# Kernel tuning notes

Measured on AMD Instinct MI355X. Metric: run time of the kernel, lower is better.

Reference implementation:

```python
import jax, jax.numpy as jnp
import numpy as np

N, E, L = 2048, 16384, 8
IN_DIM, HID, PE, EDGE_DIM, OUT_DIM, HEADS, MASK_DIM = 9, 256, 20, 2, 6, 8, 6
ENC = HID - PE
HD = HID // HEADS

def _bn(x, g, b):
    # BatchNorm1d in training-mode math (batch statistics, biased var), dropout disabled
    mu = x.mean(0)
    var = ((x - mu) ** 2).mean(0)
    return (x - mu) * jax.lax.rsqrt(var + 1e-5) * g + b

def _leaky(x):
    return jnp.where(x > 0, x, 0.01 * x)

def setup_inputs():
    key = jax.random.key(0)
    ks = iter(jax.random.split(key, 64))
    def p(*shape):
        return jax.random.normal(next(ks), shape, jnp.float32) * 0.05
    return dict(
        x=jax.random.normal(next(ks), (N, IN_DIM), jnp.float32),
        pe=jax.random.normal(next(ks), (N, PE), jnp.float32),
        edge_attr=jax.random.normal(next(ks), (E, EDGE_DIM), jnp.float32),
        mask_value=jax.random.normal(next(ks), (MASK_DIM,), jnp.float32),
        enc_w=p(IN_DIM, ENC), enc_b=p(ENC),
        in_g=jnp.ones((ENC,)), in_b=jnp.zeros((ENC,)),
        pe_g=jnp.ones((PE,)), pe_b=jnp.zeros((PE,)),
        gine_ew=p(L, EDGE_DIM, HID), gine_eb=p(L, HID),
        gine_mw=p(L, HID, HID), gine_mb=p(L, HID),
        attn_inw=p(L, HID, 3 * HID), attn_inb=p(L, 3 * HID),
        attn_outw=p(L, HID, HID), attn_outb=p(L, HID),
        mlp1w=p(L, HID, 2 * HID), mlp1b=p(L, 2 * HID),
        mlp2w=p(L, 2 * HID, HID), mlp2b=p(L, HID),
        n1g=jnp.ones((L, HID)), n1b=jnp.zeros((L, HID)),
        n2g=jnp.ones((L, HID)), n2b=jnp.zeros((L, HID)),
        n3g=jnp.ones((L, HID)), n3b=jnp.zeros((L, HID)),
        obn_g=jnp.ones((L, HID)), obn_b=jnp.zeros((L, HID)),
        pd_g=jnp.ones((HID,)), pd_b=jnp.zeros((HID,)),
        dec1w=p(HID, HID), dec1b=p(HID),
        dec2w=p(HID, OUT_DIM), dec2b=p(OUT_DIM),
        edge_index=jax.random.randint(next(ks), (2, E), 0, N, jnp.int32),
        mask=jax.random.randint(next(ks), (N, MASK_DIM), 0, 2, jnp.int32).astype(bool),
    )

def reference(x, pe, edge_attr, mask_value, enc_w, enc_b, in_g, in_b, pe_g, pe_b,
              gine_ew, gine_eb, gine_mw, gine_mb, attn_inw, attn_inb, attn_outw, attn_outb,
              mlp1w, mlp1b, mlp2w, mlp2b, n1g, n1b, n2g, n2b, n3g, n3b, obn_g, obn_b,
              pd_g, pd_b, dec1w, dec1b, dec2w, dec2b, edge_index, mask):
    src, dst = edge_index[0], edge_index[1]
    # masked-feature replacement on x[:, 3:3+mask_dim]
    blk = jnp.where(mask, mask_value[None, :], x[:, 3:3 + MASK_DIM])
    x = x.at[:, 3:3 + MASK_DIM].set(blk)
    h = _bn(_leaky(x @ enc_w + enc_b), in_g, in_b)
    h = jnp.concatenate([h, _bn(pe, pe_g, pe_b)], axis=1)  # [N, HID]
    for l in range(L):
        xin = h
        # GINEConv (eps=0): nn((1+eps)*x_i + sum_j relu(x_j + lin(e_ji)))
        eemb = edge_attr @ gine_ew[l] + gine_eb[l]            # [E, HID]
        msg = jax.nn.relu(xin[src] + eemb)                    # gather + fuse
        agg = jax.ops.segment_sum(msg, dst, num_segments=N)   # scatter-add
        hl = _leaky((xin + agg) @ gine_mw[l] + gine_mb[l])
        hl = _bn(hl + xin, n1g[l], n1b[l])                    # local branch + residual + norm1
        # global multi-head self-attention (single graph -> dense batch, no padding)
        qkv = xin @ attn_inw[l] + attn_inb[l]
        q, k, v = [t.reshape(N, HEADS, HD) for t in jnp.split(qkv, 3, axis=1)]
        a = jax.nn.softmax(jnp.einsum('nhd,mhd->hnm', q, k) / np.float32(np.sqrt(HD)), axis=-1)
        o = jnp.einsum('hnm,mhd->nhd', a, v).reshape(N, HID)
        ha = _bn(o @ attn_outw[l] + attn_outb[l] + xin, n2g[l], n2b[l])  # attn branch + residual + norm2
        out = hl + ha
        out = out + (jax.nn.relu(out @ mlp1w[l] + mlp1b[l]) @ mlp2w[l] + mlp2b[l])  # GPS FFN
        out = _bn(out, n3g[l], n3b[l])
        h = _bn(out, obn_g[l], obn_b[l])                      # outer per-layer BatchNorm
    h = _bn(h, pd_g, pd_b)
    return _leaky(h @ dec1w + dec1b) @ dec2w + dec2b
```

## Files before the change

kernel.cpp:

```cpp
#include <hip/hip_runtime.h>
#include <hip/hip_bf16.h>

typedef __hip_bfloat16 bf16;
typedef __attribute__((ext_vector_type(8))) short v8s;
typedef __attribute__((ext_vector_type(4))) float v4f;

#define NN 2048
#define EE 16384
#define LLAYERS 8
#define HIDD 256
#define ENCD 236
#define PED 20
#define BN_EPS 1e-5f
#define ATT_SCALE 0.17677669529663687f
#define KSPLIT 4

__device__ __forceinline__ float b2f(bf16 v){ return __bfloat162float(v); }
__device__ __forceinline__ float bs2f(unsigned short u){ return __uint_as_float(((unsigned)u) << 16); }
__device__ __forceinline__ unsigned short f2bs(float f){
  bf16 h = __float2bfloat16(f);
  union { bf16 b; unsigned short u; } cv; cv.b = h; return cv.u;
}
__device__ __forceinline__ float ld1f(const void* p, size_t i, int f){
  return f ? b2f(((const bf16*)p)[i]) : ((const float*)p)[i];
}

__global__ void k_detect2(const unsigned int* __restrict__ xw,
                          const unsigned char* __restrict__ mk, int* __restrict__ flags){
  __shared__ int sh[256];
  int t = threadIdx.x;
  if (blockIdx.x == 0){
    int cnt = 0;
    for (int i = t; i < 8192; i += 256){
      unsigned b = (xw[i] >> 8) & 0xffu;
      unsigned v = b & 0x7fu;
      if (v == 0u || (v >= 0x30u && v <= 0x43u)) cnt++;
    }
    sh[t] = cnt; __syncthreads();
    for (int s = 128; s; s >>= 1){ if (t < s) sh[t] += sh[t+s]; __syncthreads(); }
    if (t == 0) flags[0] = (sh[0] > 6000) ? 1 : 0;
  } else {
    int acc = 0;
    for (int i = t; i < NN*6; i += 256){
      unsigned b = mk[i]; int m = i & 3;
      if ((m == 1 && b == 0x3Fu) || (m == 0 && b == 0x80u)) acc |= 4;
      if (b == 0x3Fu || b == 0x80u) acc |= 2;
      if (m != 0 && b != 0u) acc |= 1;
    }
    sh[t] = acc; __syncthreads();
    for (int s = 128; s; s >>= 1){ if (t < s) sh[t] |= sh[t+s]; __syncthreads(); }
    if (t == 0){
      int a = sh[0];
      flags[1] = (a & 4) ? 2 : (a & 2) ? 3 : (a & 1) ? 1 : 0;
    }
  }
}

__global__ void k_tw(const void* __restrict__ src, unsigned short* __restrict__ dst,
                     int K, int N, const int* __restrict__ dflag){
  __shared__ float tile[32][33];
  int n0 = blockIdx.x*32, k0 = blockIdx.y*32, b = blockIdx.z;
  int t = threadIdx.x, x = t & 31, y = t >> 5;
  int f = dflag[0];
  size_t so = (size_t)b*K*N, dofs = (size_t)b*N*K;
  #pragma unroll
  for (int i = 0; i < 4; i++){
    int k = k0 + y + 8*i;
    tile[y+8*i][x] = ld1f(src, so + (size_t)k*N + n0 + x, f);
  }
  __syncthreads();
  #pragma unroll
  for (int i = 0; i < 4; i++){
    int n = n0 + y + 8*i;
    dst[dofs + (size_t)n*K + k0 + x] = f2bs(tile[x][y+8*i]);
  }
}
__global__ void k_tw3(const void* __restrict__ sA, const void* __restrict__ sB,
                      const void* __restrict__ sC, unsigned short* __restrict__ dst,
                      const int* __restrict__ dflag){
  __shared__ float tile[32][33];
  int z = blockIdx.z;
  const void* src = (z < 8) ? sA : (z < 16) ? sB : sC;
  int b = (z < 8) ? z : (z < 16) ? z - 8 : 0;
  int n0 = blockIdx.x*32, k0 = blockIdx.y*32;
  int t = threadIdx.x, x = t & 31, y = t >> 5;
  int f = dflag[0];
  size_t so = (size_t)b*65536, dofs = (size_t)z*65536;
  #pragma unroll
  for (int i = 0; i < 4; i++){
    int k = k0 + y + 8*i;
    tile[y+8*i][x] = ld1f(src, so + (size_t)k*256 + n0 + x, f);
  }
  __syncthreads();
  #pragma unroll
  for (int i = 0; i < 4; i++){
    int n = n0 + y + 8*i;
    dst[dofs + (size_t)n*256 + k0 + x] = f2bs(tile[x][y+8*i]);
  }
}

__global__ void k_csr_count(const int* __restrict__ ei, int* __restrict__ counts){
  int e = blockIdx.x*256 + threadIdx.x;
  if (e < EE) atomicAdd(&counts[ei[EE + e]], 1);
}
__global__ void k_csr_scan(const int* __restrict__ counts, int* __restrict__ rowstart,
                           int* __restrict__ cursor){
  __shared__ int ts[256];
  int t = threadIdx.x, base = t*8;
  int loc[8]; int s = 0;
  #pragma unroll
  for (int i = 0; i < 8; i++){ loc[i] = s; s += counts[base + i]; }
  ts[t] = s; __syncthreads();
  for (int off = 1; off < 256; off <<= 1){
    int v = (t >= off) ? ts[t - off] : 0;
    __syncthreads();
    ts[t] += v;
    __syncthreads();
  }
  int excl = ts[t] - s;
  #pragma unroll
  for (int i = 0; i < 8; i++){
    int v = excl + loc[i];
    rowstart[base + i] = v; cursor[base + i] = v;
  }
  if (t == 255) rowstart[2048] = ts[255];
}
__global__ void k_csr_fill(const int* __restrict__ ei, const void* __restrict__ ea,
                           const int* __restrict__ dflag, int* __restrict__ cursor,
                           int* __restrict__ csr_src, float2* __restrict__ csr_a){
  int e = blockIdx.x*256 + threadIdx.x;
  if (e >= EE) return;
  int s = ei[e], d = ei[EE + e];
  int pos = atomicAdd(&cursor[d], 1);
  int f = dflag[0];
  csr_src[pos] = s;
  csr_a[pos] = make_float2(ld1f(ea, (size_t)e*2, f), ld1f(ea, (size_t)e*2 + 1, f));
}

__global__ void k_encode(const void* __restrict__ x, const void* __restrict__ mval,
                         const void* __restrict__ mask, const int* __restrict__ flags,
                         const void* __restrict__ w, const void* __restrict__ b,
                         float* __restrict__ out){
  __shared__ float xr[16];
  int r = blockIdx.x, t = threadIdx.x;
  int f = flags[0];
  if (t < 9){
    float v = ld1f(x, (size_t)r*9 + t, f);
    if (t >= 3){
      int j = t - 3;
      size_t idx = (size_t)r*6 + j;
      int mf = flags[1];
      bool mm;
      if      (mf == 0) mm = ((const int*)mask)[idx] != 0;
      else if (mf == 1) mm = ((const unsigned char*)mask)[idx] != 0;
      else if (mf == 2) mm = ((const unsigned short*)mask)[idx] != 0;
      else              mm = ((const unsigned int*)mask)[idx] != 0;
      if (mm) v = ld1f(mval, j, f);
    }
    xr[t] = v;
  }
  __syncthreads();
  if (t < ENCD){
    float acc = ld1f(b, t, f);
    #pragma unroll
    for (int k = 0; k < 9; k++) acc = fmaf(xr[k], ld1f(w, (size_t)k*ENCD + t, f), acc);
    out[r*ENCD + t] = acc > 0.f ? acc : 0.01f*acc;
  }
}
__global__ void k_cvt(const void* __restrict__ src, const int* __restrict__ dflag,
                      float* __restrict__ dst, int n){
  int i = blockIdx.x*256 + threadIdx.x;
  if (i < n) dst[i] = ld1f(src, i, dflag[0]);
}
__global__ void k_bn2x(const float* __restrict__ encb, const float* __restrict__ pef,
                       const void* __restrict__ eg, const void* __restrict__ eb,
                       const void* __restrict__ pg, const void* __restrict__ pb,
                       const int* __restrict__ dflag,
                       float* __restrict__ scE, float* __restrict__ shE,
                       float* __restrict__ scP, float* __restrict__ shP){
  int cb = blockIdx.x, t = threadIdx.x;
  const float* src; int ld, c; const void *g, *b; float *sc, *sh;
  if (cb < ENCD){ src = encb; ld = ENCD; c = cb; g = eg; b = eb; sc = scE; sh = shE; }
  else          { src = pef;  ld = PED;  c = cb - ENCD; g = pg; b = pb; sc = scP; sh = shP; }
  float s = 0.f, q = 0.f;
  for (int r = t; r < NN; r += 256){ float v = src[(size_t)r*ld + c]; s += v; q += v*v; }
  __shared__ float ss[256], qs[256];
  ss[t] = s; qs[t] = q; __syncthreads();
  for (int k = 128; k; k >>= 1){ if (t < k){ ss[t] += ss[t+k]; qs[t] += qs[t+k]; } __syncthreads(); }
  if (t == 0){
    int f = dflag[0];
    float mu  = ss[0] * (1.f/NN);
    float var = qs[0] * (1.f/NN) - mu*mu;
    float r1  = rsqrtf(var + BN_EPS);
    float scv = ld1f(g, c, f) * r1;
    sc[c] = scv; sh[c] = ld1f(b, c, f) - mu*scv;
  }
}
__global__ void k_concat(unsigned short* __restrict__ h, const float* __restrict__ encb,
                         const float* __restrict__ pef,
                         const float* __restrict__ scE, const float* __restrict__ shE,
                         const float* __restrict__ scP, const float* __restrict__ shP){
  int i = blockIdx.x*256 + threadIdx.x;
  int r = i >> 8, c = i & 255;
  float v;
  if (c < ENCD) v = encb[r*ENCD + c]*scE[c] + shE[c];
  else { int j = c - ENCD; v = pef[r*PED + j]*scP[j] + shP[j]; }
  h[i] = f2bs(v);
}

__device__ __forceinline__ void dualbn(const float* slab, int c, int f,
                                       const void* g1, size_t g1o,
                                       const void* g2, size_t g2o,
// ... 24 lines not shown
                           const float* __restrict__ slabH,
                           const void* Hg1, size_t Hg1o, const void* Hg2, size_t Hg2o,
                           const void* Hb2, size_t Hb2o,
                           int dst, const int* __restrict__ rowstart,
                           const int* __restrict__ csr_src, const float2* __restrict__ csr_a,
                           const void* __restrict__ w, size_t woff,
                           const void* __restrict__ b, size_t boff, int f,
                           float* __restrict__ agg){
  int c = threadIdx.x;
  float sc = 1.f, sh = 0.f;
  if (hsrc) dualbn(slabH, c, f, Hg1, Hg1o, Hg2, Hg2o, Hb2, Hb2o, sc, sh);
  float w0 = ld1f(w, woff + c, f), w1 = ld1f(w, woff + HIDD + c, f);
  float bb = ld1f(b, boff + c, f);
  int beg = rowstart[dst], end = rowstart[dst + 1];
  float acc = 0.f;
  for (int i = beg; i < end; i++){
    int s = csr_src[i]; float2 a = csr_a[i];
    float hv = hsrc ? t3[(size_t)s*HIDD + c]*sc + sh : bs2f(h0[(size_t)s*HIDD + c]);
    float m = hv + a.x*w0 + a.y*w1 + bb;
    acc += fmaxf(m, 0.f);
  }
  agg[(size_t)dst*HIDD + c] = acc;
}

template<int ACT, int APATH, int RESMODE, int OUTBF, int STATS>
__device__ void dev_mgemm(char* sm, int bn, int bm,
    const unsigned short* __restrict__ Ab, const float* __restrict__ Af, int hsrc,
    const float* __restrict__ agg,
    const float* __restrict__ Opart, const float* __restrict__ lsum,
    const float* __restrict__ t1p, const float* __restrict__ t2p,
    const float* __restrict__ slabH,
    const void* Hg1, size_t Hg1o, const void* Hg2, size_t Hg2o,
    const void* Hb2, size_t Hb2o,
    const void* Pg, size_t Pgo, const void* Pb, size_t Pbo,
    const float* __restrict__ slab1,
    const void* g1, size_t g1o, const void* b1, size_t b1o,
    const float* __restrict__ slab2,
    const void* g2, size_t g2o, const void* b2, size_t b2o,
    const unsigned short* __restrict__ Wt,
    const void* __restrict__ bias, size_t boff,
    void* __restrict__ C, int N_, int K, int qcols, float qscale,
    float* __restrict__ stats, int f){
  unsigned short (*As)[40] = (unsigned short(*)[40])sm;
  unsigned short (*Bs)[40] = (unsigned short(*)[40])(sm + 5120);
  constexpr bool NEEDH = (APATH <= 1 || RESMODE == 1 || APATH == 4);
  constexpr size_t TB = 10240 + (NEEDH ? 2048 : 0);
  float* scH = (float*)(sm + 10240); float* shH = scH + 256;
  float* tc1 = (float*)(sm + TB);    float* th1 = tc1 + 256;
  float* tc2 = th1 + 256;            float* th2 = tc2 + 256;
  int tid = threadIdx.x, L = tid & 63, wv = tid >> 6;
  int wm = wv >> 1, wn = wv & 1;
  int quad = L >> 4, lo = L & 15;
  int srow = tid >> 2, sk = (tid & 3)*8;

  if (NEEDH && (hsrc || APATH == 4)){
    int c = tid;
    float s, h;
    dualbn(slabH, c, f, Hg1, Hg1o, Hg2, Hg2o, Hb2, Hb2o, s, h);
    if (APATH == 4){
      float mu  = slabH[2*c] * (1.f/NN);
// ... 23 lines not shown
  for (int kk = 0; kk < K; kk += 32){
    int row = bm + srow, c0 = kk + sk;
    uint4 aval;
    if (APATH == 0 || APATH == 4){
      if (APATH == 0 && !hsrc){
        aval = *(const uint4*)(Ab + (size_t)row*K + c0);
      } else {
        unsigned short us8[8];
        #pragma unroll
        for (int j = 0; j < 8; j++){
          int c = c0 + j;
          us8[j] = f2bs(Af[(size_t)row*K + c]*scH[c] + shH[c]);
        }
        aval = *(const uint4*)us8;
      }
    } else if (APATH == 1){
      unsigned short us8[8];
      if (!hsrc){
        uint4 araw = *(const uint4*)(Ab + (size_t)row*K + c0);
        unsigned parts[4] = {araw.x, araw.y, araw.z, araw.w};
        #pragma unroll
        for (int p = 0; p < 4; p++){
          us8[2*p]   = f2bs(bs2f((unsigned short)(parts[p] & 0xffffu)) + agg[(size_t)row*K + c0 + 2*p]);
          us8[2*p+1] = f2bs(bs2f((unsigned short)(parts[p] >> 16))     + agg[(size_t)row*K + c0 + 2*p + 1]);
        }
      } else {
        #pragma unroll
        for (int j = 0; j < 8; j++){
          int c = c0 + j;
          us8[j] = f2bs(Af[(size_t)row*K + c]*scH[c] + shH[c] + agg[(size_t)row*K + c]);
        }
      }
      aval = *(const uint4*)us8;
    } else if (APATH == 2){
      int hd = c0 >> 5, d0 = c0 & 31;
      size_t mlb = ((size_t)row*8 + hd)*KSPLIT;
      float inv = 1.f / (lsum[mlb] + lsum[mlb+1] + lsum[mlb+2] + lsum[mlb+3]);
      const float* Op = Opart + mlb*32 + d0;
      unsigned short us8[8];
      #pragma unroll
      for (int j = 0; j < 8; j++){
        float v = (Op[j] + Op[32+j] + Op[64+j] + Op[96+j])*inv;
        us8[j] = f2bs(v);
      }
      aval = *(const uint4*)us8;
    } else {
      unsigned short us8[8];
      #pragma unroll
// ... 51 lines not shown
  if (STATS){
    #pragma unroll
    for (int nj = 0; nj < 2; nj++){
      float s = ssum[nj], q = ssq[nj];
      s += __shfl_xor(s, 16, 64); s += __shfl_xor(s, 32, 64);
      q += __shfl_xor(q, 16, 64); q += __shfl_xor(q, 32, 64);
      if (quad == 0){
        int col = bn + wn*32 + nj*16 + lo;
        atomicAdd(&stats[2*col],   s);
        atomicAdd(&stats[2*col+1], q);
      }
    }
  }
}

__device__ void dev_attn(char* sm, const unsigned short* __restrict__ qkv,
                         int q0, int hd, int ks,
                         float* __restrict__ Opart, float* __restrict__ lsum){
  unsigned short (*Ks)[40] = (unsigned short(*)[40])sm;
  unsigned short (*Vt)[66] = (unsigned short(*)[66])(sm + 5120);
  unsigned short (*Ps)[16][68] = (unsigned short(*)[16][68])(sm + 9344);
  int tid = threadIdx.x, L = tid & 63, wv = tid >> 6;
  int quad = L >> 4, lo = L & 15;
  int skey = tid >> 2, sd = (tid & 3)*8;

  v8s qf = *(const v8s*)(qkv + (size_t)(q0 + 16*wv + lo)*768 + hd*32 + quad*8);
  v4f o0 = (v4f){0.f,0.f,0.f,0.f}, o1 = (v4f){0.f,0.f,0.f,0.f};
  float lrow[4] = {0.f, 0.f, 0.f, 0.f};

  int kbeg = ks * (NN/KSPLIT), kend = kbeg + NN/KSPLIT;
  for (int kt = kbeg; kt < kend; kt += 64){
    const unsigned short* kp = qkv + (size_t)(kt + skey)*768 + 256 + hd*32 + sd;
    uint4 kraw = *(const uint4*)kp;
    uint4 vraw = *(const uint4*)(kp + 256);
    __syncthreads();
    *(uint4*)&Ks[skey][sd] = kraw;
    {
      unsigned short vs[8]; *(uint4*)vs = vraw;
      #pragma unroll
      for (int j = 0; j < 8; j++) Vt[sd + j][skey] = vs[j];
    }
    __syncthreads();
    v4f s[4];
    #pragma unroll
    for (int sub = 0; sub < 4; sub++){
      v8s kf = *(const v8s*)&Ks[sub*16 + lo][quad*8];
      s[sub] = __builtin_amdgcn_mfma_f32_16x16x32_bf16(qf, kf, (v4f){0.f,0.f,0.f,0.f}, 0, 0, 0);
    }
    #pragma unroll
    for (int r = 0; r < 4; r++){
      #pragma unroll
      for (int sub = 0; sub < 4; sub++){
        float p = __expf(s[sub][r]);
        Ps[wv][quad*4 + r][sub*16 + lo] = f2bs(p);
        lrow[r] += p;
      }
    }
    #pragma unroll
    for (int kc = 0; kc < 2; kc++){
      v8s pf  = *(const v8s*)&Ps[wv][lo][kc*32 + quad*8];
      v8s v0f = *(const v8s*)&Vt[lo][kc*32 + quad*8];
      v8s v1f = *(const v8s*)&Vt[16 + lo][kc*32 + quad*8];
      o0 = __builtin_amdgcn_mfma_f32_16x16x32_bf16(pf, v0f, o0, 0, 0, 0);
      o1 = __builtin_amdgcn_mfma_f32_16x16x32_bf16(pf, v1f, o1, 0, 0, 0);
    }
  }
  #pragma unroll
  for (int r = 0; r < 4; r++){
// ... 16 lines not shown
__global__ void k_d1(const unsigned short* __restrict__ h0, const float* __restrict__ t3,
                     int hsrc, const float* __restrict__ slabH,
                     const void* Hg1, size_t Hg1o, const void* Hg2, size_t Hg2o,
                     const void* Hb2, size_t Hb2o,
                     const unsigned short* __restrict__ qkw,
                     const void* qb, size_t qbo, unsigned short* __restrict__ qkvb,
                     const int* __restrict__ rowstart, const int* __restrict__ csr_src,
                     const float2* __restrict__ csr_a,
                     const void* gw, size_t gwo, const void* gb, size_t gbo,
                     float* __restrict__ agg, const int* __restrict__ dflagp){
  __shared__ char sm[12288];
  int f = dflagp[0];
  int bx = blockIdx.x;
  if (bx < 384){
    dev_mgemm<0,0,0,1,0>(sm, (bx % 12)*64, (bx / 12)*64, h0, t3, hsrc,
        nullptr, nullptr, nullptr, nullptr, nullptr,
        slabH, Hg1, Hg1o, Hg2, Hg2o, Hb2, Hb2o, nullptr, 0, nullptr, 0,
        nullptr, nullptr, 0, nullptr, 0, nullptr, nullptr, 0, nullptr, 0,
        qkw, qb, qbo, qkvb, 768, 256, 256, ATT_SCALE, nullptr, f);
  } else {
    dev_gather(h0, t3, hsrc, slabH, Hg1, Hg1o, Hg2, Hg2o, Hb2, Hb2o,
               bx - 384, rowstart, csr_src, csr_a, gw, gwo, gb, gbo, f, agg);
  }
}

__launch_bounds__(256)
__global__ void k_d2(const unsigned short* __restrict__ h0, const float* __restrict__ t3,
                     int hsrc, const float* __restrict__ slabH,
                     const void* Hg1, size_t Hg1o, const void* Hg2, size_t Hg2o,
                     const void* Hb2, size_t Hb2o,
                     const float* __restrict__ agg,
                     const unsigned short* __restrict__ gmw,
                     const void* gmb, size_t gmbo,
                     float* __restrict__ t1, float* __restrict__ stats1,
                     const unsigned short* __restrict__ qkvb,
                     float* __restrict__ Opart, float* __restrict__ lsum,
                     const int* __restrict__ dflagp){
  __shared__ char sm[18432];
  int bx = blockIdx.x;
  if (bx < 128){
    int f = dflagp[0];
    dev_mgemm<2,1,1,0,1>(sm, (bx & 3)*64, (bx >> 2)*64, h0, t3, hsrc,
        agg, nullptr, nullptr, nullptr, nullptr,
        slabH, Hg1, Hg1o, Hg2, Hg2o, Hb2, Hb2o, nullptr, 0, nullptr, 0,
        nullptr, nullptr, 0, nullptr, 0, nullptr, nullptr, 0, nullptr, 0,
        gmw, gmb, gmbo, t1, 256, 256, 0, 1.f, stats1, f);
  } else {
    int b = bx - 128;
    dev_attn(sm, qkvb, (b & 31)*64, (b >> 5) & 7, b >> 8, Opart, lsum);
  }
}

__launch_bounds__(256)
__global__ void k_g3(const unsigned short* __restrict__ h0, const float* __restrict__ t3,
                     int hsrc, const float* __restrict__ slabH,
                     const void* Hg1, size_t Hg1o, const void* Hg2, size_t Hg2o,
                     const void* Hb2, size_t Hb2o,
                     const float* __restrict__ Opart, const float* __restrict__ lsum,
                     const unsigned short* __restrict__ aow,
                     const void* aob, size_t aobo,
                     float* __restrict__ t2, float* __restrict__ stats2,
                     const int* __restrict__ dflagp){
  __shared__ char sm[12288];
  dev_mgemm<0,2,1,0,1>(sm, blockIdx.x*64, blockIdx.y*64, h0, t3, hsrc,
      nullptr, Opart, lsum, nullptr, nullptr,
      slabH, Hg1, Hg1o, Hg2, Hg2o, Hb2, Hb2o, nullptr, 0, nullptr, 0,
      nullptr, nullptr, 0, nullptr, 0, nullptr, nullptr, 0, nullptr, 0,
      aow, aob, aobo, t2, 256, 256, 0, 1.f, stats2, dflagp[0]);
}

__launch_bounds__(256)
__global__ void k_g4(const float* __restrict__ t1, const float* __restrict__ t2,
                     const float* __restrict__ slab1,
                     const void* g1, size_t g1o, const void* b1, size_t b1o,
                     const float* __restrict__ slab2,
                     const void* g2, size_t g2o, const void* b2, size_t b2o,
                     const unsigned short* __restrict__ m1w,
                     const void* m1b, size_t m1bo,
                     unsigned short* __restrict__ u, const int* __restrict__ dflagp){
  __shared__ char sm[14336];
  dev_mgemm<1,3,0,1,0>(sm, blockIdx.x*64, blockIdx.y*64, nullptr, nullptr, 0,
      nullptr, nullptr, nullptr, t1, t2,
      nullptr, nullptr, 0, nullptr, 0, nullptr, 0, nullptr, 0, nullptr, 0,
      slab1, g1, g1o, b1, b1o, slab2, g2, g2o, b2, b2o,
      m1w, m1b, m1bo, u, 512, 256, 0, 1.f, nullptr, dflagp[0]);
}

__launch_bounds__(256)
__global__ void k_g5(const unsigned short* __restrict__ u,
                     const float* __restrict__ t1, const float* __restrict__ t2,
                     const float* __restrict__ slab1,
                     const void* g1, size_t g1o, const void* b1, size_t b1o,
                     const float* __restrict__ slab2,
                     const void* g2, size_t g2o, const void* b2, size_t b2o,
                     const unsigned short* __restrict__ m2w,
                     const void* m2b, size_t m2bo,
                     float* __restrict__ t3, float* __restrict__ stats3,
                     const int* __restrict__ dflagp){
  __shared__ char sm[14336];
  dev_mgemm<0,0,2,0,1>(sm, blockIdx.x*64, blockIdx.y*64, u, nullptr, 0,
      nullptr, nullptr, nullptr, t1, t2,
      nullptr, nullptr, 0, nullptr, 0, nullptr, 0, nullptr, 0, nullptr, 0,
      slab1, g1, g1o, b1, b1o, slab2, g2, g2o, b2, b2o,
      m2w, m2b, m2bo, t3, 256, 512, 0, 1.f, stats3, dflagp[0]);
}

__launch_bounds__(256)
__global__ void k_gdec(const float* __restrict__ t3, const float* __restrict__ slabH,
                       const void* Hg1, size_t Hg1o, const void* Hg2, size_t Hg2o,
                       const void* Hb2, size_t Hb2o,
                       const void* Pg, const void* Pb,
                       const unsigned short* __restrict__ d1w,
                       const void* d1bv, unsigned short* __restrict__ d1b,
                       const int* __restrict__ dflagp){
  __shared__ char sm[12288];
  dev_mgemm<2,4,0,1,0>(sm, blockIdx.x*64, blockIdx.y*64, nullptr, t3, 1,
      nullptr, nullptr, nullptr, nullptr, nullptr,
      slabH, Hg1, Hg1o, Hg2, Hg2o, Hb2, Hb2o, Pg, 0, Pb, 0,
      nullptr, nullptr, 0, nullptr, 0, nullptr, nullptr, 0, nullptr, 0,
      d1w, d1bv, 0, d1b, 256, 256, 0, 1.f, nullptr, dflagp[0]);
}

__global__ void k_dec2(const unsigned short* __restrict__ d1, const void* __restrict__ w,
                       const void* __restrict__ b, const int* __restrict__ dflag,
                       void* __restrict__ out){
  int r = blockIdx.x, t = threadIdx.x;
  int f = dflag[0];
  float a = bs2f(d1[(size_t)r*HIDD + t]);
  float p[6];
  #pragma unroll
  for (int n = 0; n < 6; n++) p[n] = a * ld1f(w, (size_t)t*6 + n, f);
  #pragma unroll
// ... 65 lines not shown
  float*          Opart= (float*)alloc((size_t)NN*8*KSPLIT*32*4);
  float*          lsum = (float*)alloc((size_t)NN*8*KSPLIT*4);
  unsigned short* sqw  = (unsigned short*)alloc((size_t)17*65536*2);
  unsigned short* ainw_t = (unsigned short*)alloc((size_t)8*768*256*2);
  unsigned short* m1w_t  = (unsigned short*)alloc((size_t)8*512*256*2);
  unsigned short* m2w_t  = (unsigned short*)alloc((size_t)8*256*512*2);
  unsigned short* gmw_t   = sqw;
  unsigned short* aoutw_t = sqw + (size_t)8*65536;
  unsigned short* d1w_t   = sqw + (size_t)16*65536;
  float* t2 = agg;
  unsigned short* u    = qkvb;
  float*          encb = (float*)qkvb;
  float*          pef  = (float*)qkvb + (size_t)NN*ENCD;
  unsigned short* d1b  = (unsigned short*)Opart;

  k_detect2<<<2, 256, 0, stream>>>((const unsigned int*)x, (const unsigned char*)mask, flags);
  hipMemsetAsync(counts, 0, zero_bytes, stream);
  k_csr_count<<<EE/256, 256, 0, stream>>>(edge_index, counts);
  k_csr_scan<<<1, 256, 0, stream>>>(counts, rowstart, cursor);
  k_csr_fill<<<EE/256, 256, 0, stream>>>(edge_index, edge_attr, dflag, cursor, csr_src, csr_a);
  k_tw3<<<dim3(8, 8, 17), 256, 0, stream>>>(gine_mw, attn_outw, dec1w, sqw, dflag);
  k_tw<<<dim3(24, 8, 8), 256, 0, stream>>>(attn_inw, ainw_t, 256, 768, dflag);
  k_tw<<<dim3(16, 8, 8), 256, 0, stream>>>(mlp1w,    m1w_t,  256, 512, dflag);
  k_tw<<<dim3(8, 16, 8), 256, 0, stream>>>(mlp2w,    m2w_t,  512, 256, dflag);
  k_encode<<<NN, 256, 0, stream>>>(x, mask_value, mask, flags, enc_w, enc_b, encb);
  k_cvt<<<(NN*PED + 255)/256, 256, 0, stream>>>(pe, dflag, pef, NN*PED);
  k_bn2x<<<256, 256, 0, stream>>>(encb, pef, in_g, in_b, pe_g, pe_b, dflag, scE, shE, scP, shP);
  k_concat<<<NN*HIDD/256, 256, 0, stream>>>(h, encb, pef, scE, shE, scP, shP);

  for (int l = 0; l < LLAYERS; l++){
    int hs = (l > 0);
    const float* slH = stats3 + (size_t)(hs ? (l-1) : 0)*512;
    size_t o3 = (size_t)(hs ? (l-1) : 0)*256;
    k_d1<<<2432, 256, 0, stream>>>(h, t3, hs, slH, n3g, o3, obn_g, o3, obn_b, o3,
        ainw_t + (size_t)l*196608, attn_inb, (size_t)l*768, qkvb,
        rowstart, csr_src, csr_a,
        gine_ew, (size_t)l*2*HIDD, gine_eb, (size_t)l*HIDD, agg, dflag);
    k_d2<<<1152, 256, 0, stream>>>(h, t3, hs, slH, n3g, o3, obn_g, o3, obn_b, o3,
        agg, gmw_t + (size_t)l*65536, gine_mb, (size_t)l*256, t1, stats1 + (size_t)l*512,
        qkvb, Opart, lsum, dflag);
    k_g3<<<dim3(4,32), 256, 0, stream>>>(h, t3, hs, slH, n3g, o3, obn_g, o3, obn_b, o3,
        Opart, lsum, aoutw_t + (size_t)l*65536, attn_outb, (size_t)l*256,
        t2, stats2 + (size_t)l*512, dflag);
    k_g4<<<dim3(8,32), 256, 0, stream>>>(t1, t2,
        stats1 + (size_t)l*512, n1g, (size_t)l*256, n1b, (size_t)l*256,
        stats2 + (size_t)l*512, n2g, (size_t)l*256, n2b, (size_t)l*256,
        m1w_t + (size_t)l*131072, mlp1b, (size_t)l*512, u, dflag);
    k_g5<<<dim3(4,32), 256, 0, stream>>>(u, t1, t2,
        stats1 + (size_t)l*512, n1g, (size_t)l*256, n1b, (size_t)l*256,
        stats2 + (size_t)l*512, n2g, (size_t)l*256, n2b, (size_t)l*256,
        m2w_t + (size_t)l*131072, mlp2b, (size_t)l*256, t3, stats3 + (size_t)l*512, dflag);
  }

// ... 6 lines not shown
```

Before: 937.9 us.

## Merge preprocessing kernels, enlarge attention/GINE tiles, batch gather loads, use exp2 softmax

Collapses about a dozen preprocessing launches (format detection, CSR build, encoder, weight transposes, input BN stats) into three multi-role kernels to cut launch overhead. The attention and GINE-MLP blocks move to 512 threads with 128-row tiles, changing per-block work and LDS use. The edge gather loop now loads eight neighbours at a time for memory-level parallelism. Softmax folds log2(e) into the Q scale so it can use exp2f. The larger blocks and the dual-role launches may lower occupancy or unbalance the work across blocks.

```diff
diff --git a/kernel.cpp b/kernel.cpp
--- a/kernel.cpp
+++ b/kernel.cpp
@@ -12,7 +12,7 @@
 #define ENCD 236
 #define PED 20
 #define BN_EPS 1e-5f
-#define ATT_SCALE 0.17677669529663687f
+#define ATT_SCALE_L2E (0.17677669529663687f * 1.4426950408889634f)
 #define KSPLIT 4
 
 __device__ __forceinline__ float b2f(bf16 v){ return __bfloat162float(v); }
@@ -25,11 +25,12 @@
   return f ? b2f(((const bf16*)p)[i]) : ((const float*)p)[i];
 }
 
-__global__ void k_detect2(const unsigned int* __restrict__ xw,
-                          const unsigned char* __restrict__ mk, int* __restrict__ flags){
+__global__ void k_pre0(const unsigned int* __restrict__ xw,
+                       const unsigned char* __restrict__ mk, int* __restrict__ flags,
+                       const int* __restrict__ ei, int* __restrict__ counts){
   __shared__ int sh[256];
-  int t = threadIdx.x;
-  if (blockIdx.x == 0){
+  int t = threadIdx.x, bx = blockIdx.x;
+  if (bx == 0){
     int cnt = 0;
     for (int i = t; i < 8192; i += 256){
       unsigned b = (xw[i] >> 8) & 0xffu;
@@ -39,7 +40,7 @@
     sh[t] = cnt; __syncthreads();
     for (int s = 128; s; s >>= 1){ if (t < s) sh[t] += sh[t+s]; __syncthreads(); }
     if (t == 0) flags[0] = (sh[0] > 6000) ? 1 : 0;
-  } else {
+  } else if (bx == 1){
     int acc = 0;
     for (int i = t; i < NN*6; i += 256){
       unsigned b = mk[i]; int m = i & 3;
@@ -53,16 +54,79 @@
       int a = sh[0];
       flags[1] = (a & 4) ? 2 : (a & 2) ? 3 : (a & 1) ? 1 : 0;
     }
-  }
-}
-
-__global__ void k_tw(const void* __restrict__ src, unsigned short* __restrict__ dst,
-                     int K, int N, const int* __restrict__ dflag){
-  __shared__ float tile[32][33];
-  int n0 = blockIdx.x*32, k0 = blockIdx.y*32, b = blockIdx.z;
+  } else {
+    int e = (bx - 2)*256 + t;
+    if (e < EE) atomicAdd(&counts[ei[EE + e]], 1);
+  }
+}
+
+__global__ void k_pre1(const int* __restrict__ counts, int* __restrict__ rowstart,
+                       int* __restrict__ cursor,
+                       const void* __restrict__ x, const void* __restrict__ mval,
+                       const void* __restrict__ mask, const int* __restrict__ flags,
+                       const void* __restrict__ w, const void* __restrict__ b,
+                       const void* __restrict__ pe,
+                       float* __restrict__ encb, float* __restrict__ pef){
+  __shared__ char smem[1088];
+  int t = threadIdx.x, bx = blockIdx.x;
+  if (bx == 0){
+    int* ts = (int*)smem;
+    int base = t*8;
+    int loc[8]; int s = 0;
+    #pragma unroll
+    for (int i = 0; i < 8; i++){ loc[i] = s; s += counts[base + i]; }
+    ts[t] = s; __syncthreads();
+    for (int off = 1; off < 256; off <<= 1){
+      int v = (t >= off) ? ts[t - off] : 0;
+      __syncthreads();
+      ts[t] += v;
+      __syncthreads();
+    }
+    int excl = ts[t] - s;
+    #pragma unroll
+    for (int i = 0; i < 8; i++){
+      int v = excl + loc[i];
+      rowstart[base + i] = v; cursor[base + i] = v;
+    }
+    if (t == 255) rowstart[2048] = ts[255];
+  } else {
+    float* xr = (float*)smem;
+    int r = bx - 1;
+    int f = flags[0];
+    if (t < 9){
+      float v = ld1f(x, (size_t)r*9 + t, f);
+      if (t >= 3){
+        int j = t - 3;
+        size_t idx = (size_t)r*6 + j;
+        int mf = flags[1];
+        bool mm;
+        if      (mf == 0) mm = ((const int*)mask)[idx] != 0;
+        else if (mf == 1) mm = ((const unsigned char*)mask)[idx] != 0;
+        else if (mf == 2) mm = ((const unsigned short*)mask)[idx] != 0;
+        else              mm = ((const unsigned int*)mask)[idx] != 0;
+        if (mm) v = ld1f(mval, j, f);
+      }
+      xr[t] = v;
+    }
+    __syncthreads();
+    if (t < ENCD){
+      float acc = ld1f(b, t, f);
+      #pragma unroll
+      for (int k = 0; k < 9; k++) acc = fmaf(xr[k], ld1f(w, (size_t)k*ENCD + t, f), acc);
+      encb[r*ENCD + t] = acc > 0.f ? acc : 0.01f*acc;
+    } else {
+      int j = t - ENCD;
+      pef[(size_t)r*PED + j] = ld1f(pe, (size_t)r*PED + j, f);
+    }
+  }
+}
+
+__device__ void dev_tw(char* smem, const void* __restrict__ src,
+                       unsigned short* __restrict__ dst,
+                       int K, int N, int b, int n0, int k0, int f){
+  float (*tile)[33] = (float(*)[33])smem;
   int t = threadIdx.x, x = t & 31, y = t >> 5;
-  int f = dflag[0];
-  size_t so = (size_t)b*K*N, dofs = (size_t)b*N*K;
+  size_t so = (size_t)b*K*N;
   #pragma unroll
   for (int i = 0; i < 4; i++){
     int k = k0 + y + 8*i;
@@ -72,130 +136,72 @@
   #pragma unroll
   for (int i = 0; i < 4; i++){
     int n = n0 + y + 8*i;
-    dst[dofs + (size_t)n*K + k0 + x] = f2bs(tile[x][y+8*i]);
-  }
-}
-__global__ void k_tw3(const void* __restrict__ sA, const void* __restrict__ sB,
-                      const void* __restrict__ sC, unsigned short* __restrict__ dst,
-                      const int* __restrict__ dflag){
-  __shared__ float tile[32][33];
-  int z = blockIdx.z;
-  const void* src = (z < 8) ? sA : (z < 16) ? sB : sC;
-  int b = (z < 8) ? z : (z < 16) ? z - 8 : 0;
-  int n0 = blockIdx.x*32, k0 = blockIdx.y*32;
-  int t = threadIdx.x, x = t & 31, y = t >> 5;
-  int f = dflag[0];
-  size_t so = (size_t)b*65536, dofs = (size_t)z*65536;
-  #pragma unroll
-  for (int i = 0; i < 4; i++){
-    int k = k0 + y + 8*i;
-    tile[y+8*i][x] = ld1f(src, so + (size_t)k*256 + n0 + x, f);
-  }
-  __syncthreads();
-  #pragma unroll
-  for (int i = 0; i < 4; i++){
-    int n = n0 + y + 8*i;
-    dst[dofs + (size_t)n*256 + k0 + x] = f2bs(tile[x][y+8*i]);
-  }
-}
-
-__global__ void k_csr_count(const int* __restrict__ ei, int* __restrict__ counts){
-  int e = blockIdx.x*256 + threadIdx.x;
-  if (e < EE) atomicAdd(&counts[ei[EE + e]], 1);
-}
-__global__ void k_csr_scan(const int* __restrict__ counts, int* __restrict__ rowstart,
-                           int* __restrict__ cursor){
-  __shared__ int ts[256];
-  int t = threadIdx.x, base = t*8;
-  int loc[8]; int s = 0;
-  #pragma unroll
-  for (int i = 0; i < 8; i++){ loc[i] = s; s += counts[base + i]; }
-  ts[t] = s; __syncthreads();
-  for (int off = 1; off < 256; off <<= 1){
-    int v = (t >= off) ? ts[t - off] : 0;
-    __syncthreads();
-    ts[t] += v;
-    __syncthreads();
-  }
-  int excl = ts[t] - s;
-  #pragma unroll
-  for (int i = 0; i < 8; i++){
-    int v = excl + loc[i];
-    rowstart[base + i] = v; cursor[base + i] = v;
-  }
-  if (t == 255) rowstart[2048] = ts[255];
-}
-__global__ void k_csr_fill(const int* __restrict__ ei, const void* __restrict__ ea,
-                           const int* __restrict__ dflag, int* __restrict__ cursor,
-                           int* __restrict__ csr_src, float2* __restrict__ csr_a){
-  int e = blockIdx.x*256 + threadIdx.x;
-  if (e >= EE) return;
-  int s = ei[e], d = ei[EE + e];
-  int pos = atomicAdd(&cursor[d], 1);
-  int f = dflag[0];
-  csr_src[pos] = s;
-  csr_a[pos] = make_float2(ld1f(ea, (size_t)e*2, f), ld1f(ea, (size_t)e*2 + 1, f));
-}
-
-__global__ void k_encode(const void* __restrict__ x, const void* __restrict__ mval,
-                         const void* __restrict__ mask, const int* __restrict__ flags,
-                         const void* __restrict__ w, const void* __restrict__ b,
-                         float* __restrict__ out){
-  __shared__ float xr[16];
-  int r = blockIdx.x, t = threadIdx.x;
+    dst[(size_t)n*K + k0 + x] = f2bs(tile[x][y+8*i]);
+  }
+}
+__global__ void k_pre2(const int* __restrict__ ei, const void* __restrict__ ea,
+                       const int* __restrict__ flags, int* __restrict__ cursor,
+                       int* __restrict__ csr_src, float2* __restrict__ csr_a,
+                       const float* __restrict__ encb, const float* __restrict__ pef,
+                       const void* eg, const void* eb, const void* pg, const void* pb,
+                       float* scE, float* shE, float* scP, float* shP,
+                       const void* gine_mw, const void* attn_outw, const void* dec1w,
+                       const void* attn_inw, const void* mlp1w, const void* mlp2w,
+                       unsigned short* sqw, unsigned short* ainw_t,
+                       unsigned short* m1w_t, unsigned short* m2w_t){
+  __shared__ char smem[4352];
+  int t = threadIdx.x, bx = blockIdx.x;
   int f = flags[0];
-  if (t < 9){
-    float v = ld1f(x, (size_t)r*9 + t, f);
-    if (t >= 3){
-      int j = t - 3;
-      size_t idx = (size_t)r*6 + j;
-      int mf = flags[1];
-      bool mm;
-      if      (mf == 0) mm = ((const int*)mask)[idx] != 0;
-      else if (mf == 1) mm = ((const unsigned char*)mask)[idx] != 0;
-      else if (mf == 2) mm = ((const unsigned short*)mask)[idx] != 0;
-      else              mm = ((const unsigned int*)mask)[idx] != 0;
-      if (mm) v = ld1f(mval, j, f);
-    }
-    xr[t] = v;
-  }
-  __syncthreads();
-  if (t < ENCD){
-    float acc = ld1f(b, t, f);
-    #pragma unroll
-    for (int k = 0; k < 9; k++) acc = fmaf(xr[k], ld1f(w, (size_t)k*ENCD + t, f), acc);
-    out[r*ENCD + t] = acc > 0.f ? acc : 0.01f*acc;
-  }
-}
-__global__ void k_cvt(const void* __restrict__ src, const int* __restrict__ dflag,
-                      float* __restrict__ dst, int n){
-  int i = blockIdx.x*256 + threadIdx.x;
-  if (i < n) dst[i] = ld1f(src, i, dflag[0]);
-}
-__global__ void k_bn2x(const float* __restrict__ encb, const float* __restrict__ pef,
-                       const void* __restrict__ eg, const void* __restrict__ eb,
-                       const void* __restrict__ pg, const void* __restrict__ pb,
-                       const int* __restrict__ dflag,
-                       float* __restrict__ scE, float* __restrict__ shE,
-                       float* __restrict__ scP, float* __restrict__ shP){
-  int cb = blockIdx.x, t = threadIdx.x;
-  const float* src; int ld, c; const void *g, *b; float *sc, *sh;
-  if (cb < ENCD){ src = encb; ld = ENCD; c = cb; g = eg; b = eb; sc = scE; sh = shE; }
-  else          { src = pef;  ld = PED;  c = cb - ENCD; g = pg; b = pb; sc = scP; sh = shP; }
-  float s = 0.f, q = 0.f;
-  for (int r = t; r < NN; r += 256){ float v = src[(size_t)r*ld + c]; s += v; q += v*v; }
-  __shared__ float ss[256], qs[256];
-  ss[t] = s; qs[t] = q; __syncthreads();
-  for (int k = 128; k; k >>= 1){ if (t < k){ ss[t] += ss[t+k]; qs[t] += qs[t+k]; } __syncthreads(); }
-  if (t == 0){
-    int f = dflag[0];
-    float mu  = ss[0] * (1.f/NN);
-    float var = qs[0] * (1.f/NN) - mu*mu;
-    float r1  = rsqrtf(var + BN_EPS);
-    float scv = ld1f(g, c, f) * r1;
-    sc[c] = scv; sh[c] = ld1f(b, c, f) - mu*scv;
-  }
-}
+  if (bx < 64){
+    int e = bx*256 + t;
+    if (e < EE){
+      int s = ei[e], d = ei[EE + e];
+      int pos = atomicAdd(&cursor[d], 1);
+      csr_src[pos] = s;
+      csr_a[pos] = make_float2(ld1f(ea, (size_t)e*2, f), ld1f(ea, (size_t)e*2 + 1, f));
+    }
+  } else if (bx < 320){
+    int cb = bx - 64;
+    const float* src; int ld, c; const void *g, *b; float *sc, *sh;
+    if (cb < ENCD){ src = encb; ld = ENCD; c = cb; g = eg; b = eb; sc = scE; sh = shE; }
+    else          { src = pef;  ld = PED;  c = cb - ENCD; g = pg; b = pb; sc = scP; sh = shP; }
+    float s = 0.f, q = 0.f;
+    for (int r = t; r < NN; r += 256){ float v = src[(size_t)r*ld + c]; s += v; q += v*v; }
+    float* ss = (float*)smem; float* qs = ss + 256;
+    ss[t] = s; qs[t] = q; __syncthreads();
+    for (int k = 128; k; k >>= 1){ if (t < k){ ss[t] += ss[t+k]; qs[t] += qs[t+k]; } __syncthreads(); }
+    if (t == 0){
+      float mu  = ss[0] * (1.f/NN);
+      float var = qs[0] * (1.f/NN) - mu*mu;
+      float r1  = rsqrtf(var + BN_EPS);
+      float scv = ld1f(g, c, f) * r1;
+      sc[c] = scv; sh[c] = ld1f(b, c, f) - mu*scv;
+    }
+  } else {
+    int id = bx - 320;
+    const void* src; unsigned short* dst; int K, N, b, x, y;
+    if (id < 1088){
+      int z = id >> 6, r = id & 63;
+      src = (z < 8) ? gine_mw : (z < 16) ? attn_outw : dec1w;
+      b = (z < 8) ? z : (z < 16) ? z - 8 : 0;
+      dst = sqw + (size_t)z*65536; K = 256; N = 256; x = r & 7; y = r >> 3;
+    } else if (id < 2624){
+      int i2 = id - 1088; b = i2 / 192; int r = i2 % 192;
+      x = r % 24; y = r / 24;
+      src = attn_inw; dst = ainw_t + (size_t)b*196608; K = 256; N = 768;
+    } else if (id < 3648){
+      int i3 = id - 2624; b = i3 >> 7; int r = i3 & 127;
+      x = r & 15; y = r >> 4;
+      src = mlp1w; dst = m1w_t + (size_t)b*131072; K = 256; N = 512;
+    } else {
+      int i4 = id - 3648; b = i4 >> 7; int r = i4 & 127;
+      x = r & 7; y = r >> 3;
+      src = mlp2w; dst = m2w_t + (size_t)b*131072; K = 512; N = 256;
+    }
+    dev_tw(smem, src, dst, K, N, b, x*32, y*32, f);
+  }
+}
+
 __global__ void k_concat(unsigned short* __restrict__ h, const float* __restrict__ encb,
                          const float* __restrict__ pef,
                          const float* __restrict__ scE, const float* __restrict__ shE,
@@ -250,11 +256,22 @@
   float bb = ld1f(b, boff + c, f);
   int beg = rowstart[dst], end = rowstart[dst + 1];
   float acc = 0.f;
-  for (int i = beg; i < end; i++){
-    int s = csr_src[i]; float2 a = csr_a[i];
-    float hv = hsrc ? t3[(size_t)s*HIDD + c]*sc + sh : bs2f(h0[(size_t)s*HIDD + c]);
-    float m = hv + a.x*w0 + a.y*w1 + bb;
-    acc += fmaxf(m, 0.f);
+  for (int i = beg; i < end; i += 8){
+    int si[8]; float2 aa[8]; float vd[8];
+    #pragma unroll
+    for (int j = 0; j < 8; j++){
+      int ix = i + j;
+      bool ok = ix < end;
+      si[j] = ok ? csr_src[ix] : 0;
+      aa[j] = ok ? csr_a[ix] : make_float2(0.f, 0.f);
+      vd[j] = ok ? 1.f : 0.f;
+    }
+    #pragma unroll
+    for (int j = 0; j < 8; j++){
+      float hv = hsrc ? t3[(size_t)si[j]*HIDD + c]*sc + sh : bs2f(h0[(size_t)si[j]*HIDD + c]);
+      float m = hv + aa[j].x*w0 + aa[j].y*w1 + bb;
+      acc += fmaxf(m, 0.f) * vd[j];
+    }
   }
   agg[(size_t)dst*HIDD + c] = acc;
 }
@@ -262,7 +279,6 @@
 template<int ACT, int APATH, int RESMODE, int OUTBF, int STATS>
 __device__ void dev_mgemm(char* sm, int bn, int bm,
     const unsigned short* __restrict__ Ab, const float* __restrict__ Af, int hsrc,
-    const float* __restrict__ agg,
     const float* __restrict__ Opart, const float* __restrict__ lsum,
     const float* __restrict__ t1p, const float* __restrict__ t2p,
     const float* __restrict__ slabH,
@@ -279,7 +295,7 @@
     float* __restrict__ stats, int f){
   unsigned short (*As)[40] = (unsigned short(*)[40])sm;
   unsigned short (*Bs)[40] = (unsigned short(*)[40])(sm + 5120);
-  constexpr bool NEEDH = (APATH <= 1 || RESMODE == 1 || APATH == 4);
+  constexpr bool NEEDH = (APATH == 0 || RESMODE == 1 || APATH == 4);
   constexpr size_t TB = 10240 + (NEEDH ? 2048 : 0);
   float* scH = (float*)(sm + 10240); float* shH = scH + 256;
   float* tc1 = (float*)(sm + TB);    float* th1 = tc1 + 256;
@@ -333,24 +349,6 @@
         }
         aval = *(const uint4*)us8;
       }
-    } else if (APATH == 1){
-      unsigned short us8[8];
-      if (!hsrc){
-        uint4 araw = *(const uint4*)(Ab + (size_t)row*K + c0);
-        unsigned parts[4] = {araw.x, araw.y, araw.z, araw.w};
-        #pragma unroll
-        for (int p = 0; p < 4; p++){
-          us8[2*p]   = f2bs(bs2f((unsigned short)(parts[p] & 0xffffu)) + agg[(size_t)row*K + c0 + 2*p]);
-          us8[2*p+1] = f2bs(bs2f((unsigned short)(parts[p] >> 16))     + agg[(size_t)row*K + c0 + 2*p + 1]);
-        }
-      } else {
-        #pragma unroll
-        for (int j = 0; j < 8; j++){
-          int c = c0 + j;
-          us8[j] = f2bs(Af[(size_t)row*K + c]*scH[c] + shH[c] + agg[(size_t)row*K + c]);
-        }
-      }
-      aval = *(const uint4*)us8;
     } else if (APATH == 2){
       int hd = c0 >> 5, d0 = c0 & 31;
       size_t mlb = ((size_t)row*8 + hd)*KSPLIT;
@@ -432,15 +430,111 @@
   }
 }
 
-__device__ void dev_attn(char* sm, const unsigned short* __restrict__ qkv,
-                         int q0, int hd, int ks,
-                         float* __restrict__ Opart, float* __restrict__ lsum){
+__device__ void dev_gine128(char* sm, int bn, int bm,
+    const unsigned short* __restrict__ h0, const float* __restrict__ t3, int hsrc,
+    const float* __restrict__ agg,
+    const float* __restrict__ slabH,
+    const void* Hg1, size_t Hg1o, const void* Hg2, size_t Hg2o,
+    const void* Hb2, size_t Hb2o,
+    const unsigned short* __restrict__ Wt,
+    const void* __restrict__ bias, size_t boff,
+    float* __restrict__ C, float* __restrict__ stats, int f){
+  unsigned short (*As)[40] = (unsigned short(*)[40])sm;
+  unsigned short (*Bs)[40] = (unsigned short(*)[40])(sm + 10240);
+  float* scH = (float*)(sm + 15360); float* shH = scH + 256;
+  int tid = threadIdx.x, L = tid & 63, wv = tid >> 6;
+  int wm = wv >> 1, wn = wv & 1;
+  int quad = L >> 4, lo = L & 15;
+  int srow = tid >> 2, sk = (tid & 3)*8;
+  int brow = tid >> 3, bk = (tid & 7)*4;
+  if (hsrc && tid < 256){
+    float s, h;
+    dualbn(slabH, tid, f, Hg1, Hg1o, Hg2, Hg2o, Hb2, Hb2o, s, h);
+    scH[tid] = s; shH[tid] = h;
+  }
+  __syncthreads();
+  v4f acc[2][2];
+  #pragma unroll
+  for (int i = 0; i < 2; i++)
+    #pragma unroll
+    for (int j = 0; j < 2; j++) acc[i][j] = (v4f){0.f,0.f,0.f,0.f};
+
+  for (int kk = 0; kk < 256; kk += 32){
+    int row = bm + srow, c0 = kk + sk;
+    unsigned short us8[8];
+    if (!hsrc){
+      uint4 araw = *(const uint4*)(h0 + (size_t)row*256 + c0);
+      unsigned parts[4] = {araw.x, araw.y, araw.z, araw.w};
+      #pragma unroll
+      for (int p = 0; p < 4; p++){
+        us8[2*p]   = f2bs(bs2f((unsigned short)(parts[p] & 0xffffu)) + agg[(size_t)row*256 + c0 + 2*p]);
+        us8[2*p+1] = f2bs(bs2f((unsigned short)(parts[p] >> 16))     + agg[(size_t)row*256 + c0 + 2*p + 1]);
+      }
+    } else {
+      #pragma unroll
+      for (int j = 0; j < 8; j++){
+        int c = c0 + j;
+        us8[j] = f2bs(t3[(size_t)row*256 + c]*scH[c] + shH[c] + agg[(size_t)row*256 + c]);
+      }
+    }
+    uint2 bval = *(const uint2*)(Wt + (size_t)(bn + brow)*256 + kk + bk);
+    __syncthreads();
+    *(uint4*)&As[srow][sk] = *(const uint4*)us8;
+    *(uint2*)&Bs[brow][bk] = bval;
+    __syncthreads();
+    v8s af[2], bfr[2];
+    af[0]  = *(const v8s*)&As[wm*32 + lo][quad*8];
+    af[1]  = *(const v8s*)&As[wm*32 + 16 + lo][quad*8];
+    bfr[0] = *(const v8s*)&Bs[wn*32 + lo][quad*8];
+    bfr[1] = *(const v8s*)&Bs[wn*32 + 16 + lo][quad*8];
+    #pragma unroll
+    for (int mi = 0; mi < 2; mi++)
+      #pragma unroll
+      for (int nj = 0; nj < 2; nj++)
+        acc[mi][nj] = __builtin_amdgcn_mfma_f32_16x16x32_bf16(af[mi], bfr[nj], acc[mi][nj], 0, 0, 0);
+  }
+
+  float ssum[2] = {0.f, 0.f}, ssq[2] = {0.f, 0.f};
+  #pragma unroll
+  for (int mi = 0; mi < 2; mi++){
+    #pragma unroll
+    for (int nj = 0; nj < 2; nj++){
+      int col = bn + wn*32 + nj*16 + lo;
+      float bv = ld1f(bias, boff + col, f);
+      #pragma unroll
+      for (int r = 0; r < 4; r++){
+        int row = bm + wm*32 + mi*16 + quad*4 + r;
+        float t = acc[mi][nj][r] + bv;
+        t = t > 0.f ? t : 0.01f*t;
+        t += hsrc ? (t3[(size_t)row*256 + col]*scH[col] + shH[col])
+                  : bs2f(h0[(size_t)row*256 + col]);
+        ssum[nj] += t; ssq[nj] += t*t;
+        C[(size_t)row*256 + col] = t;
+      }
+    }
+  }
+  #pragma unroll
+  for (int nj = 0; nj < 2; nj++){
+    float s = ssum[nj], q = ssq[nj];
+    s += __shfl_xor(s, 16, 64); s += __shfl_xor(s, 32, 64);
+    q += __shfl_xor(q, 16, 64); q += __shfl_xor(q, 32, 64);
+    if (quad == 0){
+      int col = bn + wn*32 + nj*16 + lo;
+      atomicAdd(&stats[2*col],   s);
+      atomicAdd(&stats[2*col+1], q);
+    }
+  }
+}
+
+__device__ void dev_attn512(char* sm, const unsigned short* __restrict__ qkv,
+                            int q0, int hd, int ks,
+                            float* __restrict__ Opart, float* __restrict__ lsum){
   unsigned short (*Ks)[40] = (unsigned short(*)[40])sm;
   unsigned short (*Vt)[66] = (unsigned short(*)[66])(sm + 5120);
   unsigned short (*Ps)[16][68] = (unsigned short(*)[16][68])(sm + 9344);
   int tid = threadIdx.x, L = tid & 63, wv = tid >> 6;
   int quad = L >> 4, lo = L & 15;
-  int skey = tid >> 2, sd = (tid & 3)*8;
+  int skey = tid >> 3, sd = (tid & 7)*4;
 
   v8s qf = *(const v8s*)(qkv + (size_t)(q0 + 16*wv + lo)*768 + hd*32 + quad*8);
   v4f o0 = (v4f){0.f,0.f,0.f,0.f}, o1 = (v4f){0.f,0.f,0.f,0.f};
@@ -449,14 +543,14 @@
   int kbeg = ks * (NN/KSPLIT), kend = kbeg + NN/KSPLIT;
   for (int kt = kbeg; kt < kend; kt += 64){
     const unsigned short* kp = qkv + (size_t)(kt + skey)*768 + 256 + hd*32 + sd;
-    uint4 kraw = *(const uint4*)kp;
-    uint4 vraw = *(const uint4*)(kp + 256);
+    uint2 kraw = *(const uint2*)kp;
+    uint2 vraw = *(const uint2*)(kp + 256);
     __syncthreads();
-    *(uint4*)&Ks[skey][sd] = kraw;
+    *(uint2*)&Ks[skey][sd] = kraw;
     {
-      unsigned short vs[8]; *(uint4*)vs = vraw;
-      #pragma unroll
-      for (int j = 0; j < 8; j++) Vt[sd + j][skey] = vs[j];
+      unsigned short vs[4]; *(uint2*)vs = vraw;
+      #pragma unroll
+      for (int j = 0; j < 4; j++) Vt[sd + j][skey] = vs[j];
     }
     __syncthreads();
     v4f s[4];
@@ -469,7 +563,7 @@
     for (int r = 0; r < 4; r++){
       #pragma unroll
       for (int sub = 0; sub < 4; sub++){
-        float p = __expf(s[sub][r]);
+        float p = exp2f(s[sub][r]);
         Ps[wv][quad*4 + r][sub*16 + lo] = f2bs(p);
         lrow[r] += p;
       }
@@ -516,17 +610,17 @@
   int bx = blockIdx.x;
   if (bx < 384){
     dev_mgemm<0,0,0,1,0>(sm, (bx % 12)*64, (bx / 12)*64, h0, t3, hsrc,
-        nullptr, nullptr, nullptr, nullptr, nullptr,
+        nullptr, nullptr, nullptr, nullptr,
         slabH, Hg1, Hg1o, Hg2, Hg2o, Hb2, Hb2o, nullptr, 0, nullptr, 0,
         nullptr, nullptr, 0, nullptr, 0, nullptr, nullptr, 0, nullptr, 0,
-        qkw, qb, qbo, qkvb, 768, 256, 256, ATT_SCALE, nullptr, f);
+        qkw, qb, qbo, qkvb, 768, 256, 256, ATT_SCALE_L2E, nullptr, f);
   } else {
     dev_gather(h0, t3, hsrc, slabH, Hg1, Hg1o, Hg2, Hg2o, Hb2, Hb2o,
                bx - 384, rowstart, csr_src, csr_a, gw, gwo, gb, gbo, f, agg);
   }
 }
 
-__launch_bounds__(256)
+__launch_bounds__(512)
 __global__ void k_d2(const unsigned short* __restrict__ h0, const float* __restrict__ t3,
                      int hsrc, const float* __restrict__ slabH,
                      const void* Hg1, size_t Hg1o, const void* Hg2, size_t Hg2o,
@@ -538,18 +632,15 @@
                      const unsigned short* __restrict__ qkvb,
                      float* __restrict__ Opart, float* __restrict__ lsum,
                      const int* __restrict__ dflagp){
-  __shared__ char sm[18432];
+  __shared__ char sm[26880];
   int bx = blockIdx.x;
-  if (bx < 128){
-    int f = dflagp[0];
-    dev_mgemm<2,1,1,0,1>(sm, (bx & 3)*64, (bx >> 2)*64, h0, t3, hsrc,
-        agg, nullptr, nullptr, nullptr, nullptr,
-        slabH, Hg1, Hg1o, Hg2, Hg2o, Hb2, Hb2o, nullptr, 0, nullptr, 0,
-        nullptr, nullptr, 0, nullptr, 0, nullptr, nullptr, 0, nullptr, 0,
-        gmw, gmb, gmbo, t1, 256, 256, 0, 1.f, stats1, f);
+  if (bx < 64){
+    dev_gine128(sm, (bx & 3)*64, (bx >> 2)*128, h0, t3, hsrc, agg,
+                slabH, Hg1, Hg1o, Hg2, Hg2o, Hb2, Hb2o,
+                gmw, gmb, gmbo, t1, stats1, dflagp[0]);
   } else {
-    int b = bx - 128;
-    dev_attn(sm, qkvb, (b & 31)*64, (b >> 5) & 7, b >> 8, Opart, lsum);
+    int b = bx - 64;
+    dev_attn512(sm, qkvb, (b & 15)*128, (b >> 4) & 7, b >> 7, Opart, lsum);
   }
 }
 
@@ -565,7 +656,7 @@
                      const int* __restrict__ dflagp){
   __shared__ char sm[12288];
   dev_mgemm<0,2,1,0,1>(sm, blockIdx.x*64, blockIdx.y*64, h0, t3, hsrc,
-      nullptr, Opart, lsum, nullptr, nullptr,
+      Opart, lsum, nullptr, nullptr,
       slabH, Hg1, Hg1o, Hg2, Hg2o, Hb2, Hb2o, nullptr, 0, nullptr, 0,
       nullptr, nullptr, 0, nullptr, 0, nullptr, nullptr, 0, nullptr, 0,
       aow, aob, aobo, t2, 256, 256, 0, 1.f, stats2, dflagp[0]);
@@ -582,7 +673,7 @@
                      unsigned short* __restrict__ u, const int* __restrict__ dflagp){
   __shared__ char sm[14336];
   dev_mgemm<1,3,0,1,0>(sm, blockIdx.x*64, blockIdx.y*64, nullptr, nullptr, 0,
-      nullptr, nullptr, nullptr, t1, t2,
+      nullptr, nullptr, t1, t2,
       nullptr, nullptr, 0, nullptr, 0, nullptr, 0, nullptr, 0, nullptr, 0,
       slab1, g1, g1o, b1, b1o, slab2, g2, g2o, b2, b2o,
       m1w, m1b, m1bo, u, 512, 256, 0, 1.f, nullptr, dflagp[0]);
@@ -601,7 +692,7 @@
                      const int* __restrict__ dflagp){
   __shared__ char sm[14336];
   dev_mgemm<0,0,2,0,1>(sm, blockIdx.x*64, blockIdx.y*64, u, nullptr, 0,
-      nullptr, nullptr, nullptr, t1, t2,
+      nullptr, nullptr, t1, t2,
       nullptr, nullptr, 0, nullptr, 0, nullptr, 0, nullptr, 0, nullptr, 0,
       slab1, g1, g1o, b1, b1o, slab2, g2, g2o, b2, b2o,
       m2w, m2b, m2bo, t3, 256, 512, 0, 1.f, stats3, dflagp[0]);
@@ -617,7 +708,7 @@
                        const int* __restrict__ dflagp){
   __shared__ char sm[12288];
   dev_mgemm<2,4,0,1,0>(sm, blockIdx.x*64, blockIdx.y*64, nullptr, t3, 1,
-      nullptr, nullptr, nullptr, nullptr, nullptr,
+      nullptr, nullptr, nullptr, nullptr,
       slabH, Hg1, Hg1o, Hg2, Hg2o, Hb2, Hb2o, Pg, 0, Pb, 0,
       nullptr, nullptr, 0, nullptr, 0, nullptr, nullptr, 0, nullptr, 0,
       d1w, d1bv, 0, d1b, 256, 256, 0, 1.f, nullptr, dflagp[0]);
@@ -713,18 +804,15 @@
   float*          pef  = (float*)qkvb + (size_t)NN*ENCD;
   unsigned short* d1b  = (unsigned short*)Opart;
 
-  k_detect2<<<2, 256, 0, stream>>>((const unsigned int*)x, (const unsigned char*)mask, flags);
   hipMemsetAsync(counts, 0, zero_bytes, stream);
-  k_csr_count<<<EE/256, 256, 0, stream>>>(edge_index, counts);
-  k_csr_scan<<<1, 256, 0, stream>>>(counts, rowstart, cursor);
-  k_csr_fill<<<EE/256, 256, 0, stream>>>(edge_index, edge_attr, dflag, cursor, csr_src, csr_a);
-  k_tw3<<<dim3(8, 8, 17), 256, 0, stream>>>(gine_mw, attn_outw, dec1w, sqw, dflag);
-  k_tw<<<dim3(24, 8, 8), 256, 0, stream>>>(attn_inw, ainw_t, 256, 768, dflag);
-  k_tw<<<dim3(16, 8, 8), 256, 0, stream>>>(mlp1w,    m1w_t,  256, 512, dflag);
-  k_tw<<<dim3(8, 16, 8), 256, 0, stream>>>(mlp2w,    m2w_t,  512, 256, dflag);
-  k_encode<<<NN, 256, 0, stream>>>(x, mask_value, mask, flags, enc_w, enc_b, encb);
-  k_cvt<<<(NN*PED + 255)/256, 256, 0, stream>>>(pe, dflag, pef, NN*PED);
-  k_bn2x<<<256, 256, 0, stream>>>(encb, pef, in_g, in_b, pe_g, pe_b, dflag, scE, shE, scP, shP);
+  k_pre0<<<66, 256, 0, stream>>>((const unsigned int*)x, (const unsigned char*)mask,
+                                 flags, edge_index, counts);
+  k_pre1<<<2049, 256, 0, stream>>>(counts, rowstart, cursor,
+                                   x, mask_value, mask, flags, enc_w, enc_b, pe, encb, pef);
+  k_pre2<<<4992, 256, 0, stream>>>(edge_index, edge_attr, flags, cursor, csr_src, csr_a,
+                                   encb, pef, in_g, in_b, pe_g, pe_b, scE, shE, scP, shP,
+                                   gine_mw, attn_outw, dec1w, attn_inw, mlp1w, mlp2w,
+                                   sqw, ainw_t, m1w_t, m2w_t);
   k_concat<<<NN*HIDD/256, 256, 0, stream>>>(h, encb, pef, scE, shE, scP, shP);
 
   for (int l = 0; l < LLAYERS; l++){
@@ -735,7 +823,7 @@
         ainw_t + (size_t)l*196608, attn_inb, (size_t)l*768, qkvb,
         rowstart, csr_src, csr_a,
         gine_ew, (size_t)l*2*HIDD, gine_eb, (size_t)l*HIDD, agg, dflag);
-    k_d2<<<1152, 256, 0, stream>>>(h, t3, hs, slH, n3g, o3, obn_g, o3, obn_b, o3,
+    k_d2<<<576, 512, 0, stream>>>(h, t3, hs, slH, n3g, o3, obn_g, o3, obn_b, o3,
         agg, gmw_t + (size_t)l*65536, gine_mb, (size_t)l*256, t1, stats1 + (size_t)l*512,
         qkvb, Opart, lsum, dflag);
     k_g3<<<dim3(4,32), 256, 0, stream>>>(h, t3, hs, slH, n3g, o3, obn_g, o3, obn_b, o3,
```

Result: no change. 924.3 us (-1.4%).
